# Kernel optimization log

Hardware: AMD Instinct MI355X
Metric: run time of the kernel (lower is better)

Reference implementation:

```python
import jax, jax.numpy as jnp
import numpy as np

N_NODES = 10000

def _gcn_norm(edges, n_nodes):
    # PyG GCNConv default: add self-loops, symmetric normalization D^-1/2 A_hat D^-1/2
    src, dst = edges[0], edges[1]
    loop = jnp.arange(n_nodes, dtype=src.dtype)
    src = jnp.concatenate([src, loop])
    dst = jnp.concatenate([dst, loop])
    deg = jax.ops.segment_sum(jnp.ones_like(dst, dtype=jnp.float32), dst, num_segments=n_nodes)
    dinv = jnp.where(deg > 0, jax.lax.rsqrt(deg), 0.0)
    norm = dinv[src] * dinv[dst]  # [E + N]
    return src, dst, norm

def _gcn_layer(x, src, dst, norm, W, b):
    # linear transform, then gather -> weight -> scatter-add aggregation
    x = x @ W  # [N, F]
    msg = x[src] * norm[:, None]  # [E+N, F]
    out = jax.ops.segment_sum(msg, dst, num_segments=x.shape[0])
    return out + b

def setup_inputs() -> dict:
    key = jax.random.key(0)
    k1, k2, k3, k4 = jax.random.split(key, 4)
    d = 128
    E = 640000
    scale = 1.0 / np.sqrt(d)
    return {
        "nodes_embeddings": jax.random.normal(k1, (N_NODES, d), dtype=jnp.float32),
        "edges": jax.random.randint(k2, (2, E), 0, N_NODES, dtype=jnp.int64),
        "W1": jax.random.normal(k3, (d, d), dtype=jnp.float32) * scale,
        "b1": jnp.zeros((d,), dtype=jnp.float32),
        "W2": jax.random.normal(k4, (d, d), dtype=jnp.float32) * scale,
        "b2": jnp.zeros((d,), dtype=jnp.float32),
    }

def reference(nodes_embeddings, edges, W1, b1, W2, b2):
    src, dst, norm = _gcn_norm(edges, nodes_embeddings.shape[0])
    x = _gcn_layer(nodes_embeddings, src, dst, norm, W1, b1)
    x = _gcn_layer(x, src, dst, norm, W2, b2)
    return x
```

## Files before the change

kernel.cpp:

```cpp
#include <hip/hip_runtime.h>
#include <hip/hip_bf16.h>

#define D 128
#define NBINS 157
#define BIN_CAP 4608
#define EPB 4096

__global__ __launch_bounds__(512) void fused_gemm_scatter(
        const float* __restrict__ X, const float* __restrict__ W,
        float* __restrict__ Y,
        const int* __restrict__ src, const int* __restrict__ dst,
        int* __restrict__ binTotal, int* __restrict__ binned,
        int E, int N, int gGemm) {
    __shared__ float smem[D * D];
    int tid = threadIdx.x;

    if ((int)blockIdx.x < gGemm) {
        {
            const float4* W4 = (const float4*)W;
            float4* Ws4 = (float4*)smem;
            #pragma unroll
            for (int i = 0; i < 8; ++i)
                Ws4[tid + 512 * i] = W4[tid + 512 * i];
        }
        __syncthreads();
        const float2* Ws2 = (const float2*)smem;
        int col2 = tid & 63;
        int wv   = __builtin_amdgcn_readfirstlane(tid >> 6);
        int row0 = blockIdx.x * 32 + wv * 4;
        if (row0 >= N) return;

        const float4* xr[4];
        #pragma unroll
        for (int r = 0; r < 4; ++r) {
            int rr = row0 + r; if (rr > N - 1) rr = N - 1;
            xr[r] = (const float4*)(X + (size_t)rr * D);
        }
        float accx[4] = {0.f, 0.f, 0.f, 0.f};
        float accy[4] = {0.f, 0.f, 0.f, 0.f};
        #pragma unroll 8
        for (int kb = 0; kb < 32; ++kb) {
            float4 xv[4];
            #pragma unroll
            for (int r = 0; r < 4; ++r) xv[r] = xr[r][kb];
            #pragma unroll
            for (int kk = 0; kk < 4; ++kk) {
                float2 w = Ws2[(4 * kb + kk) * 64 + col2];
                #pragma unroll
                for (int r = 0; r < 4; ++r) {
                    float xs = ((const float*)&xv[r])[kk];
                    accx[r] = fmaf(xs, w.x, accx[r]);
                    accy[r] = fmaf(xs, w.y, accy[r]);
                }
            }
        }
        #pragma unroll
        for (int r = 0; r < 4; ++r) {
            int rr = row0 + r;
            if (rr < N)
                ((float2*)Y)[(size_t)rr * 64 + col2] = make_float2(accx[r], accy[r]);
        }
    } else {
        int* cnt   = (int*)smem;
        int* loff  = cnt + 160;
        int* gbase = cnt + 320;
        int* scur  = cnt + 480;
        int* stage = cnt + 640;
        for (int b = tid; b < NBINS; b += 512) cnt[b] = 0;
        __syncthreads();

        int bid = blockIdx.x - gGemm;
        int base = bid * EPB + tid * 8;
        int s[8], dl[8], bn[8];
        int ne = 0;
        if (base + 8 <= E) {
            const int4* s4 = (const int4*)(src + base);
            const int4* d4 = (const int4*)(dst + base);
            int4 a0 = s4[0], a1 = s4[1], c0 = d4[0], c1 = d4[1];
            int ss[8] = {a0.x, a0.y, a0.z, a0.w, a1.x, a1.y, a1.z, a1.w};
            int dd[8] = {c0.x, c0.y, c0.z, c0.w, c1.x, c1.y, c1.z, c1.w};
            ne = 8;
            #pragma unroll
            for (int i = 0; i < 8; ++i) { s[i] = ss[i]; bn[i] = dd[i] >> 6; dl[i] = dd[i] & 63; }
        } else {
            for (int i = 0; i < 8; ++i) {
                int e = base + i;
                if (e < E) { s[ne] = src[e]; int d = dst[e]; bn[ne] = d >> 6; dl[ne] = d & 63; ++ne; }
            }
        }
        for (int i = 0; i < ne; ++i) atomicAdd(&cnt[bn[i]], 1);
        __syncthreads();

        if (tid < NBINS) gbase[tid] = atomicAdd(&binTotal[tid], cnt[tid]);
        if (tid < 64) {
            int c0 = (3 * tid     < NBINS) ? cnt[3 * tid    ] : 0;
            int c1 = (3 * tid + 1 < NBINS) ? cnt[3 * tid + 1] : 0;
            int c2 = (3 * tid + 2 < NBINS) ? cnt[3 * tid + 2] : 0;
            int tsum = c0 + c1 + c2;
            int incl = tsum;
            #pragma unroll
            for (int off = 1; off < 64; off <<= 1) {
                int t = __shfl_up(incl, off);
                if (tid >= off) incl += t;
            }
            int excl = incl - tsum;
            if (3 * tid     < NBINS) loff[3 * tid    ] = excl;
            if (3 * tid + 1 < NBINS) loff[3 * tid + 1] = excl + c0;
            if (3 * tid + 2 < NBINS) loff[3 * tid + 2] = excl + c0 + c1;
        }
        __syncthreads();
        if (tid < NBINS) scur[tid] = loff[tid];
        __syncthreads();

        for (int i = 0; i < ne; ++i) {
            int p = atomicAdd(&scur[bn[i]], 1);
            stage[p] = s[i] | (dl[i] << 14);
        }
        __syncthreads();

        int wv = tid >> 6, lane = tid & 63;
        for (int b = wv; b < NBINS; b += 8) {
            int n = cnt[b], so = loff[b], go = b * BIN_CAP + gbase[b];
            for (int i = lane; i < n; i += 64) binned[go + i] = stage[so + i];
        }
    }
}

__global__ __launch_bounds__(256) void sort_bins(const int* __restrict__ binTotal,
                                                 int* __restrict__ binned,
                                                 float* __restrict__ dinv,
                                                 int* __restrict__ nodeStart,
                                                 int* __restrict__ nodeEnd,
                                                 float* __restrict__ Y, int N) {
    __shared__ int h[4][64];
    __shared__ int cur[4][64];
    __shared__ float sdinv[64];
    __shared__ int stage[BIN_CAP];
    int b = blockIdx.x, tid = threadIdx.x;
    int wv = tid >> 6, lane = tid & 63;
    int cntb = binTotal[b];
    h[wv][lane] = 0;
    __syncthreads();
    const int* bp = binned + b * BIN_CAP;
    for (int i = tid; i < cntb; i += 256) atomicAdd(&h[wv][bp[i] >> 14], 1);
    __syncthreads();
    if (tid < 64) {
        int d0 = h[0][tid], d1 = h[1][tid], d2 = h[2][tid], d3 = h[3][tid];
        int deg = d0 + d1 + d2 + d3;
        int incl = deg;
        #pragma unroll
        for (int off = 1; off < 64; off <<= 1) {
            int t = __shfl_up(incl, off);
            if (tid >= off) incl += t;
        }
        int excl = incl - deg;
        cur[0][tid] = excl;
        cur[1][tid] = excl + d0;
        cur[2][tid] = excl + d0 + d1;
        cur[3][tid] = excl + d0 + d1 + d2;
        float dv = rsqrtf((float)(deg + 1));
        sdinv[tid] = dv;
        int node = b * 64 + tid;
        if (node < N) {
            dinv[node]      = dv;
            nodeStart[node] = b * BIN_CAP + excl;
            nodeEnd[node]   = b * BIN_CAP + excl + deg;
        }
    }
    __syncthreads();
    for (int i = tid; i < cntb; i += 256) {
        int p = bp[i];
        int pos = atomicAdd(&cur[wv][p >> 14], 1);
        stage[pos] = p & 0x3FFF;
    }
    {
        float4* Y4 = (float4*)Y;
        #pragma unroll
        for (int i = 0; i < 8; ++i) {
            int idx = tid + 256 * i;
            int row = idx >> 5, c = idx & 31;
            int node = b * 64 + row;
            if (node < N) {
                float4 v = Y4[(size_t)node * 32 + c];
                float dv = sdinv[row];
                v.x *= dv; v.y *= dv; v.z *= dv; v.w *= dv;
                Y4[(size_t)node * 32 + c] = v;
            }
        }
    }
    __syncthreads();
    int* bw = binned + b * BIN_CAP;
    for (int i = tid; i < cntb; i += 256) bw[i] = stage[i];
}

__global__ __launch_bounds__(256) void gemm_scale(const float* __restrict__ X,
                                                  const float* __restrict__ W,
                                                  const float* __restrict__ dinv,
                                                  float* __restrict__ Z, int N) {
    __shared__ float Ws[D * D];
    {
        const float4* W4 = (const float4*)W;
        float4* Ws4 = (float4*)Ws;
        #pragma unroll
        for (int i = 0; i < 16; ++i)
            Ws4[threadIdx.x + 256 * i] = W4[threadIdx.x + 256 * i];
    }
    __syncthreads();
    const float2* Ws2 = (const float2*)Ws;
    int col2 = threadIdx.x & 63;
    int wv   = __builtin_amdgcn_readfirstlane(threadIdx.x >> 6);
    int row0 = blockIdx.x * 16 + wv * 4;
    if (row0 >= N) return;

    const float4* xr[4];
    #pragma unroll
    for (int r = 0; r < 4; ++r) {
        int rr = row0 + r; if (rr > N - 1) rr = N - 1;
        xr[r] = (const float4*)(X + (size_t)rr * D);
    }
    float accx[4] = {0.f, 0.f, 0.f, 0.f};
    float accy[4] = {0.f, 0.f, 0.f, 0.f};
    #pragma unroll 8
    for (int kb = 0; kb < 32; ++kb) {
        float4 xv[4];
        #pragma unroll
        for (int r = 0; r < 4; ++r) xv[r] = xr[r][kb];
        #pragma unroll
        for (int kk = 0; kk < 4; ++kk) {
            float2 w = Ws2[(4 * kb + kk) * 64 + col2];
            #pragma unroll
            for (int r = 0; r < 4; ++r) {
                float xs = ((const float*)&xv[r])[kk];
                accx[r] = fmaf(xs, w.x, accx[r]);
                accy[r] = fmaf(xs, w.y, accy[r]);
            }
        }
    }
    #pragma unroll
    for (int r = 0; r < 4; ++r) {
        int rr = row0 + r;
        if (rr < N) {
            float dv = dinv[rr];
            ((float2*)Z)[(size_t)rr * 64 + col2] = make_float2(accx[r] * dv, accy[r] * dv);
        }
    }
}

__global__ __launch_bounds__(256) void aggregate(const float* __restrict__ Z,
                                                 const int* __restrict__ nodeStart,
                                                 const int* __restrict__ nodeEnd,
                                                 const int* __restrict__ csr,
                                                 const float* __restrict__ dinv,
                                                 const float* __restrict__ bias,
                                                 float* __restrict__ Out, int N) {
    int s    = blockIdx.x & 3;
    int wv   = __builtin_amdgcn_readfirstlane(threadIdx.x >> 6);
    int node = (blockIdx.x >> 2) * 4 + wv;
    if (node >= N) return;
    int lane = threadIdx.x & 63;
    int grp  = lane >> 3;
    int l8   = lane & 7;
    int off4 = s * 8 + l8;

    const float4* Z4 = (const float4*)Z;
    float ax = 0.f, ay = 0.f, az = 0.f, aw = 0.f;
    int e   = nodeStart[node];
    int end = nodeEnd[node];
    while (e < end) {
        int cnt = end - e; if (cnt > 64) cnt = 64;
        int my = (lane < cnt) ? csr[e + lane] : 0;
        if (cnt == 64) {
            #pragma unroll
            for (int j = 0; j < 8; ++j) {
                int idx = __shfl(my, j * 8 + grp);
                float4 v = Z4[idx * 32 + off4];
                ax += v.x; ay += v.y; az += v.z; aw += v.w;
            }
        } else {
            int full = cnt >> 3;
            for (int j = 0; j < full; ++j) {
                int idx = __shfl(my, j * 8 + grp);
                float4 v = Z4[idx * 32 + off4];
                ax += v.x; ay += v.y; az += v.z; aw += v.w;
            }
            int rem = cnt & 7;
            if (rem) {
                int ei = full * 8 + grp;
                int idx = __shfl(my, ei < cnt ? ei : 0);
                float4 v = Z4[idx * 32 + off4];
                if (grp < rem) { ax += v.x; ay += v.y; az += v.z; aw += v.w; }
            }
        }
        e += cnt;
    }
    #pragma unroll
    for (int m = 8; m <= 32; m <<= 1) {
        ax += __shfl_xor(ax, m);
        ay += __shfl_xor(ay, m);
        az += __shfl_xor(az, m);
        aw += __shfl_xor(aw, m);
    }
    if (lane < 8) {
        float4 self = Z4[node * 32 + off4];
        float dv = dinv[node];
        float4 b4 = ((const float4*)bias)[off4];
        float4 o;
        o.x = (ax + self.x) * dv + b4.x;
        o.y = (ay + self.y) * dv + b4.y;
        o.z = (az + self.z) * dv + b4.z;
        o.w = (aw + self.w) * dv + b4.w;
        ((float4*)Out)[node * 32 + off4] = o;
    }
}

extern "C" void kernel_launch(void* const* d_in, const int* in_sizes, int n_in,
                              void* d_out, int out_size, void* d_ws, size_t ws_size,
                              hipStream_t stream) {
    const float* X  = (const float*)d_in[0];
    const int*   ed = (const int*)d_in[1];
    const float* W1 = (const float*)d_in[2];
    const float* b1 = (const float*)d_in[3];
    const float* W2 = (const float*)d_in[4];
    const float* b2 = (const float*)d_in[5];
    float* out = (float*)d_out;

    const int N = in_sizes[0] / D;
    const int E = in_sizes[1] / 2;
    const int* src = ed;
    const int* dst = ed + E;

    char* w = (char*)d_ws;
    float* Z         = (float*)w;   w += (size_t)N * D * sizeof(float);
    int*   binned    = (int*)w;     w += (size_t)NBINS * BIN_CAP * sizeof(int);
    float* dinv      = (float*)w;   w += (size_t)N * sizeof(float);
    int*   nodeStart = (int*)w;     w += (size_t)N * sizeof(int);
    int*   nodeEnd   = (int*)w;     w += (size_t)N * sizeof(int);
    int*   binTotal  = (int*)w;     w += (size_t)NBINS * sizeof(int);

    hipMemsetAsync(binTotal, 0, NBINS * sizeof(int), stream);

    int gGemm1 = (N + 31) / 32;
    int gScat  = (E + EPB - 1) / EPB;
    fused_gemm_scatter<<<gGemm1 + gScat, 512, 0, stream>>>(
        X, W1, Z, src, dst, binTotal, binned, E, N, gGemm1);
    sort_bins<<<NBINS, 256, 0, stream>>>(binTotal, binned, dinv, nodeStart, nodeEnd, Z, N);

    int gAgg = ((N + 3) / 4) * 4;
    aggregate<<<gAgg, 256, 0, stream>>>(Z, nodeStart, nodeEnd, binned, dinv, b1, out, N);

    int gGemm2 = (N + 15) / 16;
    gemm_scale<<<gGemm2, 256, 0, stream>>>(out, W2, dinv, Z, N);
    aggregate<<<gAgg, 256, 0, stream>>>(Z, nodeStart, nodeEnd, binned, dinv, b2, out, N);
}
```

Baseline: 155.0 us.

## Pad per-node CSR rows to multiples of 8 with a zero dummy node and store indices as 16-bit

Each node's neighbor list is padded to a multiple of 8 entries using a sentinel index N that points at an appended zero row of Z. This removes the remainder branch in the aggregation loop. Neighbor indices are also written to a separate 16-bit CSR array, halving index traffic in both aggregate passes. The costs are extra padded gathers of the zero row, a larger BIN_CAP and workspace, and indices now limited to 16 bits.

```diff
diff --git a/kernel.cpp b/kernel.cpp
--- a/kernel.cpp
+++ b/kernel.cpp
@@ -3,7 +3,7 @@
 
 #define D 128
 #define NBINS 157
-#define BIN_CAP 4608
+#define BIN_CAP 5120
 #define EPB 4096
 
 __global__ __launch_bounds__(512) void fused_gemm_scatter(
@@ -127,7 +127,8 @@
 }
 
 __global__ __launch_bounds__(256) void sort_bins(const int* __restrict__ binTotal,
-                                                 int* __restrict__ binned,
+                                                 const int* __restrict__ binned,
+                                                 unsigned short* __restrict__ csr16,
                                                  float* __restrict__ dinv,
                                                  int* __restrict__ nodeStart,
                                                  int* __restrict__ nodeEnd,
@@ -135,6 +136,7 @@
     __shared__ int h[4][64];
     __shared__ int cur[4][64];
     __shared__ float sdinv[64];
+    __shared__ int padTot;
     __shared__ int stage[BIN_CAP];
     int b = blockIdx.x, tid = threadIdx.x;
     int wv = tid >> 6, lane = tid & 63;
@@ -147,26 +149,31 @@
     if (tid < 64) {
         int d0 = h[0][tid], d1 = h[1][tid], d2 = h[2][tid], d3 = h[3][tid];
         int deg = d0 + d1 + d2 + d3;
-        int incl = deg;
+        int pdeg = (deg + 7) & ~7;
+        int incl = pdeg;
         #pragma unroll
         for (int off = 1; off < 64; off <<= 1) {
             int t = __shfl_up(incl, off);
             if (tid >= off) incl += t;
         }
-        int excl = incl - deg;
+        int excl = incl - pdeg;
         cur[0][tid] = excl;
         cur[1][tid] = excl + d0;
         cur[2][tid] = excl + d0 + d1;
         cur[3][tid] = excl + d0 + d1 + d2;
         float dv = rsqrtf((float)(deg + 1));
         sdinv[tid] = dv;
+        if (tid == 63) padTot = incl;
         int node = b * 64 + tid;
         if (node < N) {
             dinv[node]      = dv;
             nodeStart[node] = b * BIN_CAP + excl;
-            nodeEnd[node]   = b * BIN_CAP + excl + deg;
-        }
-    }
+            nodeEnd[node]   = b * BIN_CAP + excl + pdeg;
+        }
+    }
+    __syncthreads();
+    int cntPad = padTot;
+    for (int i = tid; i < cntPad; i += 256) stage[i] = N;
     __syncthreads();
     for (int i = tid; i < cntb; i += 256) {
         int p = bp[i];
@@ -188,9 +195,13 @@
             }
         }
     }
-    __syncthreads();
-    int* bw = binned + b * BIN_CAP;
-    for (int i = tid; i < cntb; i += 256) bw[i] = stage[i];
+    if (b == 0) {
+        float4* Y4 = (float4*)Y;
+        if (tid < 32) Y4[(size_t)N * 32 + tid] = make_float4(0.f, 0.f, 0.f, 0.f);
+    }
+    __syncthreads();
+    unsigned short* bw = csr16 + b * BIN_CAP;
+    for (int i = tid; i < cntPad; i += 256) bw[i] = (unsigned short)stage[i];
 }
 
 __global__ __launch_bounds__(256) void gemm_scale(const float* __restrict__ X,
@@ -249,7 +260,7 @@
 __global__ __launch_bounds__(256) void aggregate(const float* __restrict__ Z,
                                                  const int* __restrict__ nodeStart,
                                                  const int* __restrict__ nodeEnd,
-                                                 const int* __restrict__ csr,
+                                                 const unsigned short* __restrict__ csr16,
                                                  const float* __restrict__ dinv,
                                                  const float* __restrict__ bias,
                                                  float* __restrict__ Out, int N) {
@@ -268,28 +279,13 @@
     int end = nodeEnd[node];
     while (e < end) {
         int cnt = end - e; if (cnt > 64) cnt = 64;
-        int my = (lane < cnt) ? csr[e + lane] : 0;
-        if (cnt == 64) {
-            #pragma unroll
-            for (int j = 0; j < 8; ++j) {
-                int idx = __shfl(my, j * 8 + grp);
-                float4 v = Z4[idx * 32 + off4];
-                ax += v.x; ay += v.y; az += v.z; aw += v.w;
-            }
-        } else {
-            int full = cnt >> 3;
-            for (int j = 0; j < full; ++j) {
-                int idx = __shfl(my, j * 8 + grp);
-                float4 v = Z4[idx * 32 + off4];
-                ax += v.x; ay += v.y; az += v.z; aw += v.w;
-            }
-            int rem = cnt & 7;
-            if (rem) {
-                int ei = full * 8 + grp;
-                int idx = __shfl(my, ei < cnt ? ei : 0);
-                float4 v = Z4[idx * 32 + off4];
-                if (grp < rem) { ax += v.x; ay += v.y; az += v.z; aw += v.w; }
-            }
+        int my = (lane < cnt) ? (int)csr16[e + lane] : 0;
+        int rounds = cnt >> 3;
+        #pragma unroll 8
+        for (int j = 0; j < rounds; ++j) {
+            int idx = __shfl(my, j * 8 + grp);
+            float4 v = Z4[idx * 32 + off4];
+            ax += v.x; ay += v.y; az += v.z; aw += v.w;
         }
         e += cnt;
     }
@@ -330,12 +326,13 @@
     const int* dst = ed + E;
 
     char* w = (char*)d_ws;
-    float* Z         = (float*)w;   w += (size_t)N * D * sizeof(float);
-    int*   binned    = (int*)w;     w += (size_t)NBINS * BIN_CAP * sizeof(int);
-    float* dinv      = (float*)w;   w += (size_t)N * sizeof(float);
-    int*   nodeStart = (int*)w;     w += (size_t)N * sizeof(int);
-    int*   nodeEnd   = (int*)w;     w += (size_t)N * sizeof(int);
-    int*   binTotal  = (int*)w;     w += (size_t)NBINS * sizeof(int);
+    float* Z          = (float*)w;            w += (size_t)(N + 1) * D * sizeof(float);
+    int*   binned     = (int*)w;              w += (size_t)NBINS * BIN_CAP * sizeof(int);
+    unsigned short* csr16 = (unsigned short*)w; w += (size_t)NBINS * BIN_CAP * sizeof(unsigned short);
+    float* dinv       = (float*)w;            w += (size_t)N * sizeof(float);
+    int*   nodeStart  = (int*)w;              w += (size_t)N * sizeof(int);
+    int*   nodeEnd    = (int*)w;              w += (size_t)N * sizeof(int);
+    int*   binTotal   = (int*)w;              w += (size_t)NBINS * sizeof(int);
 
     hipMemsetAsync(binTotal, 0, NBINS * sizeof(int), stream);
 
@@ -343,12 +340,13 @@
     int gScat  = (E + EPB - 1) / EPB;
     fused_gemm_scatter<<<gGemm1 + gScat, 512, 0, stream>>>(
         X, W1, Z, src, dst, binTotal, binned, E, N, gGemm1);
-    sort_bins<<<NBINS, 256, 0, stream>>>(binTotal, binned, dinv, nodeStart, nodeEnd, Z, N);
+    sort_bins<<<NBINS, 256, 0, stream>>>(binTotal, binned, csr16, dinv,
+                                         nodeStart, nodeEnd, Z, N);
 
     int gAgg = ((N + 3) / 4) * 4;
-    aggregate<<<gAgg, 256, 0, stream>>>(Z, nodeStart, nodeEnd, binned, dinv, b1, out, N);
+    aggregate<<<gAgg, 256, 0, stream>>>(Z, nodeStart, nodeEnd, csr16, dinv, b1, out, N);
 
     int gGemm2 = (N + 15) / 16;
     gemm_scale<<<gGemm2, 256, 0, stream>>>(out, W2, dinv, Z, N);
-    aggregate<<<gAgg, 256, 0, stream>>>(Z, nodeStart, nodeEnd, binned, dinv, b2, out, N);
-}
+    aggregate<<<gAgg, 256, 0, stream>>>(Z, nodeStart, nodeEnd, csr16, dinv, b2, out, N);
+}
```

After: 159.0 us. 1.03x slower.
